# Kernel tuning notes

Hardware: AMD Instinct MI355X
Metric: run time of the kernel (lower is better)

## Reference

```python
import jax, jax.numpy as jnp
import numpy as np

N = 100000      # nodes
E = 1_600_000   # edges (avg degree 16)
F = 128         # num_features
H = 128         # hidden
C = 10          # num_classes


def _agg_norm(row, col, mask, n, by_row):
    # A[dst=row, src=col]; scale rows (target) or cols (source) by mask,
    # remove any existing diagonal entries and add self-loops with value 1
    # (fill_diag(A,1.0)), then symmetric D^-1/2 A D^-1/2 normalization.
    m = mask[row] if by_row else mask[col]
    val = jnp.where(row == col, 0.0, m)              # off-diagonal edge values
    deg = jax.ops.segment_sum(val, row, num_segments=n) + 1.0  # +1 from self-loop
    dinv = deg ** -0.5                                # deg >= 1, never inf
    return dinv[row] * val * dinv[col], dinv * dinv   # edge vals, diag vals


def _spmm(val, diag, row, col, x, n):
    # y = A_hat @ x with off-diagonal edge list + explicit diagonal
    y = jax.ops.segment_sum(val[:, None] * x[col], row, num_segments=n)
    return y + diag[:, None] * x


def setup_inputs() -> dict:
    key = jax.random.key(0)
    ks = jax.random.split(key, 12)
    x = jax.random.normal(ks[0], (N, F), jnp.float32)
    src = jax.random.randint(ks[1], (E,), 0, N)
    dst = jax.random.randint(ks[2], (E,), 0, N)
    edge_index = jnp.stack([src, dst]).astype(jnp.int64)
    cc_mask = (jax.random.uniform(ks[3], (N,)) < 0.5).astype(jnp.float32)
    s = 0.05  # stand-in for xavier scale; exact init irrelevant to correctness
    W1L = jax.random.normal(ks[4], (F, H), jnp.float32) * s
    W1H = jax.random.normal(ks[5], (F, H), jnp.float32) * s
    W2L = jax.random.normal(ks[6], (H, H), jnp.float32) * s
    W2H = jax.random.normal(ks[7], (H, H), jnp.float32) * s
    WX = jax.random.normal(ks[8], (F, H), jnp.float32) * s
    lam1 = jnp.zeros((2,), jnp.float32)
    lam2 = jnp.zeros((2,), jnp.float32)
    lin_w = jax.random.normal(ks[9], (H, C), jnp.float32) * s
    lin_b = jnp.zeros((C,), jnp.float32)
    return {"x": x, "edge_index": edge_index, "cc_mask": cc_mask,
            "W1L": W1L, "W1H": W1H, "W2L": W2L, "W2H": W2H, "WX": WX,
            "lam1": lam1, "lam2": lam2, "lin_w": lin_w, "lin_b": lin_b}


def reference(x, edge_index, cc_mask, W1L, W1H, W2L, W2H, WX, lam1, lam2, lin_w, lin_b):
    n = x.shape[0]
    row = edge_index[1]   # destination (aggregation target)
    col = edge_index[0]   # source
    rev = 1.0 - cc_mask

    vl,  dl  = _agg_norm(row, col, cc_mask, n, True)    # target-masked (low)
    vll, dll = _agg_norm(row, col, cc_mask, n, False)   # source-masked (low)
    vh,  dh  = _agg_norm(row, col, rev,     n, True)    # target-masked (high)
    vhh, dhh = _agg_norm(row, col, rev,     n, False)   # source-masked (high)

    xl = jax.nn.relu(_spmm(vl, dl, row, col, x, n) @ W1L)
    xl = _spmm(vll, dll, row, col, xl, n) @ W2L

    xh = jax.nn.relu(_spmm(vh, dh, row, col, x, n) @ W1H)
    xh = _spmm(vhh, dhh, row, col, xh, n) @ W2H

    xc = x @ WX

    lamxl, laml = jax.nn.softmax(lam1)
    lamxh, lamh = jax.nn.softmax(lam2)
    lamx = lamxl * cc_mask + lamxh * rev                # per-node gate [N]

    xf = jax.nn.relu(lamx[:, None] * xc + laml * xl + lamh * xh)
    return xf @ lin_w + lin_b                           # [N, C] logits
```

## Files before the change

kernel.cpp:

```cpp
#include <hip/hip_runtime.h>
#include <stdint.h>

typedef unsigned int u32;
typedef unsigned short u16;
typedef unsigned long long u64;

#define DI __device__ __forceinline__

DI float bf2f(u16 u) { union { u32 i; float f; } v; v.i = ((u32)u) << 16; return v.f; }
DI u16 f2bf(float f) {
    union { u32 i; float f; } v; v.f = f;
    u32 u = v.i;
    u32 r = (u + 0x7fffu + ((u >> 16) & 1u)) >> 16;
    return (u16)r;
}
DI float2 unpack2(u32 x) { return make_float2(bf2f((u16)(x & 0xffffu)), bf2f((u16)(x >> 16))); }
DI u32 pack2(float a, float b) { return (u32)f2bf(a) | ((u32)f2bf(b) << 16); }

DI void fma8(float* acc, float w, uint4 xv) {
    float2 f0 = unpack2(xv.x), f1 = unpack2(xv.y), f2 = unpack2(xv.z), f3 = unpack2(xv.w);
    acc[0] += w * f0.x; acc[1] += w * f0.y; acc[2] += w * f1.x; acc[3] += w * f1.y;
    acc[4] += w * f2.x; acc[5] += w * f2.y; acc[6] += w * f3.x; acc[7] += w * f3.y;
}

DI uint4 scale8(uint4 v, float s) {
    uint4 r;
    float2 f;
    f = unpack2(v.x); r.x = pack2(f.x * s, f.y * s);
    f = unpack2(v.y); r.y = pack2(f.x * s, f.y * s);
    f = unpack2(v.z); r.z = pack2(f.x * s, f.y * s);
    f = unpack2(v.w); r.w = pack2(f.x * s, f.y * s);
    return r;
}


__global__ void pre_k(const float* __restrict__ X, u16* __restrict__ Xb, int total4, int cvtBlocks,
                      const float* __restrict__ mask, u64* __restrict__ bits, int n) {
    if ((int)blockIdx.x < cvtBlocks) {
        int i = blockIdx.x * blockDim.x + threadIdx.x;
        if (i >= total4) return;
        float4 v = ((const float4*)X)[i];
        ushort4 o;
        o.x = f2bf(v.x); o.y = f2bf(v.y); o.z = f2bf(v.z); o.w = f2bf(v.w);
        ((ushort4*)Xb)[i] = o;
    } else {
        int bid = blockIdx.x - cvtBlocks;
        int i = bid * 256 + threadIdx.x;
        bool m = (i < n) && (mask[i] != 0.f);
        u64 word = __ballot(m);
        if ((threadIdx.x & 63) == 0) {
            if (i < n) bits[i >> 6] = word;
        }
    }
}


#define CHUNK 8192
#define NBPAD 800

__global__ __launch_bounds__(256) void k_count(const int* __restrict__ ei, int E, int NB,
                                               u32* __restrict__ hist2d) {
    __shared__ u32 hist[NBPAD];
    for (int i = threadIdx.x; i < NBPAD; i += 256) hist[i] = 0;
    __syncthreads();
    int base = blockIdx.x * CHUNK;
    int end = min(base + CHUNK, E);
    for (int e = base + threadIdx.x; e < end; e += 256) {
        int c = ei[e], r = ei[E + e];
        if (r != c) atomicAdd(&hist[r >> 7], 1u);
    }
    __syncthreads();
    u32* out = hist2d + (size_t)blockIdx.x * NBPAD;
    for (int i = threadIdx.x; i < NB; i += 256) out[i] = hist[i];
}

__global__ __launch_bounds__(256) void k_colscan(const u32* __restrict__ hist2d,
                                                 u32* __restrict__ off2d,
                                                 int NBLK, u32* __restrict__ btotal) {
    __shared__ u32 s[256];
    int t = blockIdx.x;
    int k = threadIdx.x;
    u32 v = (k < NBLK) ? hist2d[(size_t)k * NBPAD + t] : 0;
    s[k] = v;
    __syncthreads();
    for (int off = 1; off < 256; off <<= 1) {
        u32 tmp = (k >= off) ? s[k - off] : 0;
        __syncthreads();
        s[k] += tmp;
        __syncthreads();
    }
    if (k < NBLK) off2d[(size_t)k * NBPAD + t] = s[k] - v;
    if (k == 0) btotal[t] = s[255];
}

__global__ __launch_bounds__(1024) void k_basescan(const u32* __restrict__ btotal,
                                                   u32* __restrict__ bbase, int NB) {
    __shared__ u32 s[1024];
    int t = threadIdx.x;
    u32 v = (t < NB) ? btotal[t] : 0;
    s[t] = v;
    __syncthreads();
    for (int off = 1; off < 1024; off <<= 1) {
        u32 tmp = (t >= off) ? s[t - off] : 0;
        __syncthreads();
        s[t] += tmp;
        __syncthreads();
    }
    if (t < NB) bbase[t] = s[t] - v;
    if (t == NB - 1) bbase[NB] = s[t];
}

__global__ __launch_bounds__(256) void k_scatter(const int* __restrict__ ei, int E, int NB,
                                                 const u32* __restrict__ off2d,
                                                 const u32* __restrict__ bbase,
                                                 const u64* __restrict__ bits,
                                                 u32* __restrict__ bentry) {
    __shared__ u32 cur[NBPAD];
    const u32* off = off2d + (size_t)blockIdx.x * NBPAD;
    for (int i = threadIdx.x; i < NB; i += 256) cur[i] = off[i] + bbase[i];
    __syncthreads();
    int base = blockIdx.x * CHUNK;
    int end = min(base + CHUNK, E);
    for (int e = base + threadIdx.x; e < end; e += 256) {
        int c = ei[e], r = ei[E + e];
        if (r != c) {
            u32 pos = atomicAdd(&cur[r >> 7], 1u);
            u32 m = (u32)((bits[c >> 6] >> (c & 63)) & 1);
            bentry[pos] = (u32)(r & 127) | ((u32)c << 7) | (m << 31);
        }
    }
}

__global__ __launch_bounds__(256) void k_rowhist(const u32* __restrict__ bentry,
                                                 const u32* __restrict__ bbase,
                                                 u32* __restrict__ cntP, int n) {
    __shared__ u32 h[128];
    if (threadIdx.x < 128) h[threadIdx.x] = 0;
    __syncthreads();
    u32 s0 = bbase[blockIdx.x], s1 = bbase[blockIdx.x + 1];
    for (u32 i = s0 + threadIdx.x; i < s1; i += 256) {
        u32 e = bentry[i];
        atomicAdd(&h[e & 127], 1u + ((e >> 31) << 16));
    }
    __syncthreads();
    int row = blockIdx.x * 128 + threadIdx.x;
    if (threadIdx.x < 128 && row < n) cntP[row] = h[threadIdx.x];
}

#define SCAN_B 1024
__global__ __launch_bounds__(1024) void scanA(const u32* __restrict__ cntP, int* __restrict__ rowptr,
                                              int* __restrict__ blocksum, int n) {
    __shared__ int s[SCAN_B];
    int t = threadIdx.x;
    int i = blockIdx.x * SCAN_B + t;
    int v = (i < n) ? (int)(cntP[i] & 0xffffu) : 0;
    s[t] = v; __syncthreads();
    for (int off = 1; off < SCAN_B; off <<= 1) {
        int tmp = (t >= off) ? s[t - off] : 0;
        __syncthreads();
        s[t] += tmp;
        __syncthreads();
    }
    if (i < n) rowptr[i] = s[t] - v;
    if (t == SCAN_B - 1) blocksum[blockIdx.x] = s[t];
}

__global__ __launch_bounds__(256) void scanBC(const int* __restrict__ blocksum, int nblk,
                                              int* __restrict__ rowptr, const u32* __restrict__ cntP,
                                              const float* __restrict__ mask,
                                              int* __restrict__ mid,
                                              float* __restrict__ dinvL, float* __restrict__ dinvH,
                                              float* __restrict__ dinvLL, float* __restrict__ dinvHH,
                                              float2* __restrict__ diag1, float2* __restrict__ diag2, int n) {
    __shared__ int s[128];
    int t = threadIdx.x;
    if (t < 128) s[t] = (t < nblk) ? blocksum[t] : 0;
    __syncthreads();
    for (int off = 1; off < 128; off <<= 1) {
        int tmp = (t >= off && t < 128) ? s[t - off] : 0;
        __syncthreads();
        if (t < 128) s[t] += tmp;
        __syncthreads();
    }
    int blockoff = (blockIdx.x == 0) ? 0 : s[blockIdx.x - 1];
    if (blockIdx.x == 0 && t == 0) rowptr[n] = s[127];
#pragma unroll
    for (int k = 0; k < 4; k++) {
        int i = blockIdx.x * SCAN_B + k * 256 + t;
        if (i >= n) break;
        int v = rowptr[i] + blockoff;
        rowptr[i] = v;
        u32 p = cntP[i];
        int ci = (int)(p & 0xffffu);
        int cmi = (int)(p >> 16);
        mid[i] = v + cmi;
        float c = (float)ci;
        float cm = (float)cmi;
        bool mi = mask[i] != 0.f;
        float degL = (mi ? c : 0.f) + 1.f;
        float degH = (mi ? 0.f : c) + 1.f;
        float degLL = cm + 1.f;
        float degHH = (c - cm) + 1.f;
        dinvL[i] = rsqrtf(degL);
        dinvH[i] = rsqrtf(degH);
        dinvLL[i] = rsqrtf(degLL);
        dinvHH[i] = rsqrtf(degHH);
        diag1[i] = make_float2(1.f / degL, 1.f / degH);
        diag2[i] = make_float2(1.f / degLL, 1.f / degHH);
    }
}

__global__ __launch_bounds__(256) void k_place(const u32* __restrict__ bentry,
                                               const u32* __restrict__ bbase,
                                               const int* __restrict__ rowptr, const int* __restrict__ mid,
                                               int* __restrict__ sorted, int n) {
    __shared__ int cur[256];
    int row = blockIdx.x * 128 + threadIdx.x;
    if (threadIdx.x < 128) {
        int rr = min(row, n - 1);
        cur[threadIdx.x] = rowptr[rr];
        cur[128 + threadIdx.x] = mid[rr];
    }
    __syncthreads();
    u32 s0 = bbase[blockIdx.x], s1 = bbase[blockIdx.x + 1];
    for (u32 i = s0 + threadIdx.x; i < s1; i += 256) {
        u32 e = bentry[i];
        int rl = e & 127;
        int col = (int)((e >> 7) & 0x1FFFF);
        int isH = (int)((e >> 31) ^ 1u);
        int pos = atomicAdd(&cur[rl + (isH << 7)], 1);
        sorted[pos] = col;
    }
}


__global__ __launch_bounds__(256) void spmm1(const u16* __restrict__ X,
                                             const int* __restrict__ rowptr, const int* __restrict__ sorted,
                                             const float* __restrict__ mask,
                                             const float* __restrict__ dinvL, const float* __restrict__ dinvH,
                                             const float2* __restrict__ diag1,
                                             u16* __restrict__ Yl, u16* __restrict__ Yh, int n) {
    int r = blockIdx.x * 4 + (threadIdx.x >> 6);
    if (r >= n) return;
    int lane = threadIdx.x & 63;
    int q = lane >> 4, l16 = lane & 15;
    bool mi = mask[r] != 0.f;
    const float* dinvA = mi ? dinvL : dinvH;
    float da = dinvA[r];
    float2 dg = diag1[r];
    float diag = mi ? dg.x : dg.y;

    const uint4* Xv = (const uint4*)X;
    uint4 xown = Xv[(size_t)r * 16 + l16];

    float acc[8] = {0.f, 0.f, 0.f, 0.f, 0.f, 0.f, 0.f, 0.f};
    int e0 = rowptr[r], e1 = rowptr[r + 1];
    int last = e1 - 1;
    for (int base = e0; base < e1; base += 8) {
        int s0 = base + q, s1 = base + 4 + q;
        int i0 = min(s0, last), i1 = min(s1, last);
        int c0 = sorted[i0], c1 = sorted[i1];
        float w0 = (s0 < e1) ? da * dinvA[c0] : 0.f;
        float w1 = (s1 < e1) ? da * dinvA[c1] : 0.f;
        uint4 x0 = Xv[(size_t)c0 * 16 + l16];
        uint4 x1 = Xv[(size_t)c1 * 16 + l16];
        fma8(acc, w0, x0);
        fma8(acc, w1, x1);
    }
#pragma unroll
    for (int k = 0; k < 8; k++) {
        acc[k] += __shfl_xor(acc[k], 16);
        acc[k] += __shfl_xor(acc[k], 32);
    }
    float2 o0 = unpack2(xown.x), o1 = unpack2(xown.y), o2 = unpack2(xown.z), o3 = unpack2(xown.w);
    uint4 res;
    res.x = pack2(acc[0] + diag * o0.x, acc[1] + diag * o0.y);
    res.y = pack2(acc[2] + diag * o1.x, acc[3] + diag * o1.y);
    res.z = pack2(acc[4] + diag * o2.x, acc[5] + diag * o2.y);
    res.w = pack2(acc[6] + diag * o3.x, acc[7] + diag * o3.y);
    uint4* Ya = (uint4*)(mi ? Yl : Yh);
    uint4* Yc = (uint4*)(mi ? Yh : Yl);
    if (q == 0) Ya[(size_t)r * 16 + l16] = res;
    if (q == 1) Yc[(size_t)r * 16 + l16] = xown;
}


__global__ __launch_bounds__(256) void spmm2(const u16* __restrict__ XL, const u16* __restrict__ XH,
                                             const int* __restrict__ rowptr, const int* __restrict__ mid,
                                             const int* __restrict__ sorted,
                                             const float* __restrict__ dinvLL, const float* __restrict__ dinvHH,
                                             const float2* __restrict__ diag2,
                                             u16* __restrict__ Zl, u16* __restrict__ Zh, int n) {
    int r = blockIdx.x * 4 + (threadIdx.x >> 6);
    if (r >= n) return;
    int lane = threadIdx.x & 63;
    int q = lane >> 4, l16 = lane & 15;

    float dllr = dinvLL[r], dhhr = dinvHH[r];
    float2 dg = diag2[r];

    const uint4* XLv = (const uint4*)XL;
    const uint4* XHv = (const uint4*)XH;
    uint4 xlown = XLv[(size_t)r * 16 + l16];
    uint4 xhown = XHv[(size_t)r * 16 + l16];

    float accL[8] = {0.f, 0.f, 0.f, 0.f, 0.f, 0.f, 0.f, 0.f};
    float accH[8] = {0.f, 0.f, 0.f, 0.f, 0.f, 0.f, 0.f, 0.f};
    int e0 = rowptr[r], m = mid[r], e1 = rowptr[r + 1];

    int lastL = m - 1;
    for (int base = e0; base < m; base += 8) {
        int s0 = base + q, s1 = base + 4 + q;
        int i0 = min(s0, lastL), i1 = min(s1, lastL);
        int c0 = sorted[i0], c1 = sorted[i1];
        float w0 = (s0 < m) ? dllr * dinvLL[c0] : 0.f;
        float w1 = (s1 < m) ? dllr * dinvLL[c1] : 0.f;
        uint4 x0 = XLv[(size_t)c0 * 16 + l16];
        uint4 x1 = XLv[(size_t)c1 * 16 + l16];
        fma8(accL, w0, x0);
        fma8(accL, w1, x1);
    }
    int lastH = e1 - 1;
    for (int base = m; base < e1; base += 8) {
        int s0 = base + q, s1 = base + 4 + q;
        int i0 = min(s0, lastH), i1 = min(s1, lastH);
        int c0 = sorted[i0], c1 = sorted[i1];
        float w0 = (s0 < e1) ? dhhr * dinvHH[c0] : 0.f;
        float w1 = (s1 < e1) ? dhhr * dinvHH[c1] : 0.f;
        uint4 x0 = XHv[(size_t)c0 * 16 + l16];
        uint4 x1 = XHv[(size_t)c1 * 16 + l16];
        fma8(accH, w0, x0);
        fma8(accH, w1, x1);
    }
#pragma unroll
    for (int k = 0; k < 8; k++) {
        accL[k] += __shfl_xor(accL[k], 16);
        accL[k] += __shfl_xor(accL[k], 32);
        accH[k] += __shfl_xor(accH[k], 16);
        accH[k] += __shfl_xor(accH[k], 32);
    }
    float2 l0 = unpack2(xlown.x), l1 = unpack2(xlown.y), l2 = unpack2(xlown.z), l3 = unpack2(xlown.w);
    float2 h0 = unpack2(xhown.x), h1 = unpack2(xhown.y), h2 = unpack2(xhown.z), h3 = unpack2(xhown.w);
    float cl = dg.x, ch = dg.y;
    uint4 rl, rh;
    rl.x = pack2(accL[0] + cl * l0.x, accL[1] + cl * l0.y);
    rl.y = pack2(accL[2] + cl * l1.x, accL[3] + cl * l1.y);
    rl.z = pack2(accL[4] + cl * l2.x, accL[5] + cl * l2.y);
    rl.w = pack2(accL[6] + cl * l3.x, accL[7] + cl * l3.y);
    rh.x = pack2(accH[0] + ch * h0.x, accH[1] + ch * h0.y);
    rh.y = pack2(accH[2] + ch * h1.x, accH[3] + ch * h1.y);
    rh.z = pack2(accH[4] + ch * h2.x, accH[5] + ch * h2.y);
    rh.w = pack2(accH[6] + ch * h3.x, accH[7] + ch * h3.y);
    if (q == 0) ((uint4*)Zl)[(size_t)r * 16 + l16] = rl;
    if (q == 1) ((uint4*)Zh)[(size_t)r * 16 + l16] = rh;
}


__global__ void transposeW(const float* __restrict__ W1L, const float* __restrict__ W1H,
                           const float* __restrict__ W2L, const float* __restrict__ W2H,
                           const float* __restrict__ WX,
                           const float* __restrict__ lam1, const float* __restrict__ lam2,
                           u16* __restrict__ Bt) {
    int w = blockIdx.x >> 6;
    int idx = (blockIdx.x & 63) * 256 + threadIdx.x;
    float scale = 1.f;
    if (w == 2) { float e0 = __expf(lam1[0]), e1 = __expf(lam1[1]); scale = e1 / (e0 + e1); }
    if (w == 3) { float f0 = __expf(lam2[0]), f1 = __expf(lam2[1]); scale = f1 / (f0 + f1); }
    const float* src = (w == 0) ? W1L : (w == 1) ? W1H : (w == 2) ? W2L : (w == 3) ? W2H : WX;
    int k = idx >> 7, nn = idx & 127;
    Bt[(size_t)w * 16384 + (size_t)nn * 128 + k] = f2bf(scale * src[idx]);
}


typedef __attribute__((ext_vector_type(8))) short bf16x8;
typedef __attribute__((ext_vector_type(4))) float f32x4;

DI void stageB(const uint4* __restrict__ Bt4, uint4* Bs, int tid) {
#pragma unroll
    for (int i = 0; i < 8; i++) {
        int g = i * 256 + tid;
        int nn = g >> 4, c = g & 15;
        int d = ((nn >> 4) * 4 + (c >> 2)) * 64 + (c & 3) * 16 + (nn & 15);
        Bs[d] = Bt4[g];
    }
}

DI void loadA(uint4* a, const uint4* __restrict__ A4, int mr, int quad) {
#pragma unroll
    for (int kb = 0; kb < 4; kb++)
        a[kb] = A4[(size_t)mr * 16 + kb * 4 + quad];
}

DI void mfmaSec(const uint4* a, const uint4* Bs, f32x4* acc, int lane) {
#pragma unroll
    for (int nt = 0; nt < 8; nt++)
#pragma unroll
        for (int kb = 0; kb < 4; kb++) {
            bf16x8 av = *(const bf16x8*)&a[kb];
            bf16x8 bv = *(const bf16x8*)&Bs[(nt * 4 + kb) * 64 + lane];
            acc[nt] = __builtin_amdgcn_mfma_f32_16x16x32_bf16(av, bv, acc[nt], 0, 0, 0);
        }
}


__global__ __launch_bounds__(256) void gemm_lds(const u16* __restrict__ A0, const u16* __restrict__ Bt0,
                                                u16* __restrict__ C0,
                                                const u16* __restrict__ A1, const u16* __restrict__ Bt1,
                                                u16* __restrict__ C1, int M) {
    __shared__ uint4 Bs[2048];
    const u16* A = blockIdx.y ? A1 : A0;
    const u16* Bt = blockIdx.y ? Bt1 : Bt0;
    u16* C = blockIdx.y ? C1 : C0;

    int tid = threadIdx.x;
    int wave = tid >> 6, lane = tid & 63, quad = lane >> 4, l16 = lane & 15;
    int tile = blockIdx.x * 64;
    int m0 = tile + wave * 16 + l16;
    int mr = min(m0, M - 1);

    uint4 a[4];
    loadA(a, (const uint4*)A, mr, quad);
    stageB((const uint4*)Bt, Bs, tid);
    __syncthreads();

    f32x4 acc[8];
#pragma unroll
    for (int nt = 0; nt < 8; nt++) acc[nt] = f32x4{0.f, 0.f, 0.f, 0.f};
    mfmaSec(a, Bs, acc, lane);

    __syncthreads();
    u16* Cs = (u16*)Bs;
    int lrow0 = wave * 16 + quad * 4;
#pragma unroll
    for (int nt = 0; nt < 8; nt++)
#pragma unroll
        for (int rr = 0; rr < 4; rr++) {
            float v = acc[nt][rr];
            v = v > 0.f ? v : 0.f;
            Cs[(lrow0 + rr) * 128 + nt * 16 + l16] = f2bf(v);
        }
    __syncthreads();
    uint4* Cs4 = (uint4*)Bs;
    uint4* C4 = (uint4*)C;
#pragma unroll
    for (int i = 0; i < 4; i++) {
        int g = i * 256 + tid;
        int grow = tile + (g >> 4);
        if (grow < M) C4[(size_t)grow * 16 + (g & 15)] = Cs4[g];
    }
}


__global__ __launch_bounds__(256) void fused_final(const u16* __restrict__ Zl, const u16* __restrict__ Zh,
                                                   const u16* __restrict__ Xb,
                                                   const u16* __restrict__ BtL, const u16* __restrict__ BtH,
                                                   const u16* __restrict__ BtX,
                                                   const float* __restrict__ mask,
                                                   const float* __restrict__ lam1, const float* __restrict__ lam2,
                                                   const float* __restrict__ lin_w, const float* __restrict__ lin_b,
                                                   float* __restrict__ out, int M) {
    __shared__ uint4 Bs[2048];
    __shared__ float lws[1280];

    int tid = threadIdx.x;
    int wave = tid >> 6, lane = tid & 63, quad = lane >> 4, l16 = lane & 15;
    int tile = blockIdx.x * 64;
    int m0 = tile + wave * 16 + l16;
    int mr = min(m0, M - 1);

    uint4 a[4], an[4];
    loadA(a, (const uint4*)Zl, mr, quad);
    {
        const uint4* lw4 = (const uint4*)lin_w;
        uint4* lws4 = (uint4*)lws;
        lws4[tid] = lw4[tid];
        if (tid < 64) lws4[256 + tid] = lw4[256 + tid];
    }
    stageB((const uint4*)BtL, Bs, tid);

    float e0 = __expf(lam1[0]), e1 = __expf(lam1[1]);
    float lamxl = e0 / (e0 + e1);
    float f0 = __expf(lam2[0]), f1 = __expf(lam2[1]);
    float lamxh = f0 / (f0 + f1);
    float lamx = (mask[mr] != 0.f) ? lamxl : lamxh;

    __syncthreads();

    f32x4 acc[8];
#pragma unroll
    for (int nt = 0; nt < 8; nt++) acc[nt] = f32x4{0.f, 0.f, 0.f, 0.f};

    loadA(an, (const uint4*)Zh, mr, quad);
    mfmaSec(a, Bs, acc, lane);

    __syncthreads();
    stageB((const uint4*)BtH, Bs, tid);
#pragma unroll
    for (int kb = 0; kb < 4; kb++) a[kb] = an[kb];
    loadA(an, (const uint4*)Xb, mr, quad);
    __syncthreads();
    mfmaSec(a, Bs, acc, lane);

    __syncthreads();
    stageB((const uint4*)BtX, Bs, tid);
#pragma unroll
    for (int kb = 0; kb < 4; kb++) a[kb] = scale8(an[kb], lamx);
    __syncthreads();
    mfmaSec(a, Bs, acc, lane);

    int rbase = tile + wave * 16 + quad * 4;
    float part[4][10];
#pragma unroll
    for (int rr = 0; rr < 4; rr++)
#pragma unroll
        for (int c = 0; c < 10; c++) part[rr][c] = 0.f;

#pragma unroll
    for (int nt = 0; nt < 8; nt++) {
        const float* lw = lws + (nt * 16 + l16) * 10;
        float lwv[10];
#pragma unroll
        for (int c = 0; c < 10; c++) lwv[c] = lw[c];
#pragma unroll
        for (int rr = 0; rr < 4; rr++) {
            float p = acc[nt][rr];
            p = p > 0.f ? p : 0.f;
#pragma unroll
            for (int c = 0; c < 10; c++) part[rr][c] += p * lwv[c];
        }
    }
#pragma unroll
    for (int rr = 0; rr < 4; rr++)
#pragma unroll
        for (int c = 0; c < 10; c++) {
            part[rr][c] += __shfl_xor(part[rr][c], 1);
            part[rr][c] += __shfl_xor(part[rr][c], 2);
            part[rr][c] += __shfl_xor(part[rr][c], 4);
            part[rr][c] += __shfl_xor(part[rr][c], 8);
        }
    if (l16 == 0) {
#pragma unroll
        for (int rr = 0; rr < 4; rr++) {
            int row = rbase + rr;
            if (row < M) {
#pragma unroll
                for (int c = 0; c < 10; c++)
                    out[(size_t)row * 10 + c] = part[rr][c] + lin_b[c];
            }
        }
    }
}


extern "C" void kernel_launch(void* const* d_in, const int* in_sizes, int n_in,
                              void* d_out, int out_size, void* d_ws, size_t ws_size,
                              hipStream_t stream) {
    const float* x = (const float*)d_in[0];
    const int* ei = (const int*)d_in[1];
    const float* mask = (const float*)d_in[2];
    const float* W1L = (const float*)d_in[3];
    const float* W1H = (const float*)d_in[4];
    const float* W2L = (const float*)d_in[5];
    const float* W2H = (const float*)d_in[6];
    const float* WX = (const float*)d_in[7];
    const float* lam1 = (const float*)d_in[8];
    const float* lam2 = (const float*)d_in[9];
    const float* lin_w = (const float*)d_in[10];
    const float* lin_b = (const float*)d_in[11];
    float* out = (float*)d_out;

    int E = in_sizes[1] / 2;
    int n = in_sizes[2];
    int NB = (n + 127) >> 7;
    int NBLK = (E + CHUNK - 1) / CHUNK;

    char* w = (char*)d_ws;
    size_t off = 0;
    auto alloc = [&](size_t bytes) -> void* {
        off = (off + 255) & ~(size_t)255;
        void* p = w + off;
        off += bytes;
        return p;
    };
    u32* cntP = (u32*)alloc((size_t)n * 4);
    u64* bits = (u64*)alloc((size_t)((n + 63) / 64 + 1) * 8);
    int* rowptr = (int*)alloc((size_t)(n + 1) * 4);
    int* midp = (int*)alloc((size_t)n * 4);
    int* blocksum = (int*)alloc(128 * 4);
    u32* hist2d = (u32*)alloc((size_t)NBLK * NBPAD * 4);
    u32* off2d = (u32*)alloc((size_t)NBLK * NBPAD * 4);
    u32* btotal = (u32*)alloc((size_t)NBPAD * 4);
    u32* bbase = (u32*)alloc((size_t)(NB + 1) * 4);
    u32* bentry = (u32*)alloc((size_t)E * 4);
    int* sorted = (int*)alloc((size_t)E * 4);
    float* dinvL = (float*)alloc((size_t)n * 4);
    float* dinvH = (float*)alloc((size_t)n * 4);
    float* dinvLL = (float*)alloc((size_t)n * 4);
    float* dinvHH = (float*)alloc((size_t)n * 4);
    float2* diag1 = (float2*)alloc((size_t)n * 8);
    float2* diag2 = (float2*)alloc((size_t)n * 8);
    u16* Bt = (u16*)alloc(5 * 16384 * 2);
    size_t actb = (size_t)n * 128 * 2;
    u16* Xb = (u16*)alloc(actb);
    u16* B0 = (u16*)alloc(actb);
    u16* B1 = (u16*)alloc(actb);
    u16* B2 = (u16*)alloc(actb);
    u16* B3 = (u16*)alloc(actb);

    int nblkScan = (n + SCAN_B - 1) / SCAN_B;
    int total4 = n * 128 / 4;
    int cvtBlocks = (total4 + 255) / 256;
    int maskBlocks = ((n + 63) / 64 + 3) / 4;

    pre_k<<<cvtBlocks + maskBlocks, 256, 0, stream>>>(x, Xb, total4, cvtBlocks, mask, bits, n);
    k_count<<<NBLK, 256, 0, stream>>>(ei, E, NB, hist2d);
    k_colscan<<<NB, 256, 0, stream>>>(hist2d, off2d, NBLK, btotal);
    k_basescan<<<1, 1024, 0, stream>>>(btotal, bbase, NB);
    k_scatter<<<NBLK, 256, 0, stream>>>(ei, E, NB, off2d, bbase, bits, bentry);
    k_rowhist<<<NB, 256, 0, stream>>>(bentry, bbase, cntP, n);
    scanA<<<nblkScan, 1024, 0, stream>>>(cntP, rowptr, blocksum, n);
    scanBC<<<nblkScan, 256, 0, stream>>>(blocksum, nblkScan, rowptr, cntP, mask, midp,
                                         dinvL, dinvH, dinvLL, dinvHH, diag1, diag2, n);
    k_place<<<NB, 256, 0, stream>>>(bentry, bbase, rowptr, midp, sorted, n);

    int rowsblk = (n + 3) / 4;
    int gemmblk = (n + 63) / 64;

    spmm1<<<rowsblk, 256, 0, stream>>>(Xb, rowptr, sorted, mask, dinvL, dinvH, diag1, B0, B1, n);
    transposeW<<<320, 256, 0, stream>>>(W1L, W1H, W2L, W2H, WX, lam1, lam2, Bt);
    gemm_lds<<<dim3(gemmblk, 2), 256, 0, stream>>>(B0, Bt + 0 * 16384, B2,
                                                   B1, Bt + 1 * 16384, B3, n);

    spmm2<<<rowsblk, 256, 0, stream>>>(B2, B3, rowptr, midp, sorted, dinvLL, dinvHH, diag2, B0, B1, n);

    fused_final<<<gemmblk, 256, 0, stream>>>(B0, B1, Xb,
                                             Bt + 2 * 16384, Bt + 3 * 16384, Bt + 4 * 16384,
                                             mask, lam1, lam2, lin_w, lin_b, out, n);
}
```

Before: 413.3 us.

## Merge preprocessing kernels into one launch and simplify SpMM gather loop

```diff
diff --git a/kernel.cpp b/kernel.cpp
--- a/kernel.cpp
+++ b/kernel.cpp
@@ -34,43 +34,61 @@
 }
 
 
-__global__ void pre_k(const float* __restrict__ X, u16* __restrict__ Xb, int total4, int cvtBlocks,
-                      const float* __restrict__ mask, u64* __restrict__ bits, int n) {
-    if ((int)blockIdx.x < cvtBlocks) {
-        int i = blockIdx.x * blockDim.x + threadIdx.x;
+#define CHUNK 8192
+#define NBPAD 800
+
+__global__ __launch_bounds__(256) void head_k(const float* __restrict__ X, u16* __restrict__ Xb,
+                                              int total4, int cvtBlocks, int maskBlocks,
+                                              const float* __restrict__ mask, u64* __restrict__ bits, int n,
+                                              const float* __restrict__ W1L, const float* __restrict__ W1H,
+                                              const float* __restrict__ W2L, const float* __restrict__ W2H,
+                                              const float* __restrict__ WX,
+                                              const float* __restrict__ lam1, const float* __restrict__ lam2,
+                                              u16* __restrict__ Bt,
+                                              const int* __restrict__ ei, int E, int NB,
+                                              u32* __restrict__ hist2d) {
+    int bx = blockIdx.x;
+    if (bx < cvtBlocks) {
+        int i = bx * 256 + threadIdx.x;
         if (i >= total4) return;
         float4 v = ((const float4*)X)[i];
         ushort4 o;
         o.x = f2bf(v.x); o.y = f2bf(v.y); o.z = f2bf(v.z); o.w = f2bf(v.w);
         ((ushort4*)Xb)[i] = o;
-    } else {
-        int bid = blockIdx.x - cvtBlocks;
-        int i = bid * 256 + threadIdx.x;
+        return;
+    }
+    bx -= cvtBlocks;
+    if (bx < maskBlocks) {
+        int i = bx * 256 + threadIdx.x;
         bool m = (i < n) && (mask[i] != 0.f);
         u64 word = __ballot(m);
-        if ((threadIdx.x & 63) == 0) {
-            if (i < n) bits[i >> 6] = word;
-        }
-    }
-}
-
-
-#define CHUNK 8192
-#define NBPAD 800
-
-__global__ __launch_bounds__(256) void k_count(const int* __restrict__ ei, int E, int NB,
-                                               u32* __restrict__ hist2d) {
+        if ((threadIdx.x & 63) == 0 && i < n) bits[i >> 6] = word;
+        return;
+    }
+    bx -= maskBlocks;
+    if (bx < 320) {
+        int w = bx >> 6;
+        int idx = (bx & 63) * 256 + threadIdx.x;
+        float scale = 1.f;
+        if (w == 2) { float e0 = __expf(lam1[0]), e1 = __expf(lam1[1]); scale = e1 / (e0 + e1); }
+        if (w == 3) { float f0 = __expf(lam2[0]), f1 = __expf(lam2[1]); scale = f1 / (f0 + f1); }
+        const float* src = (w == 0) ? W1L : (w == 1) ? W1H : (w == 2) ? W2L : (w == 3) ? W2H : WX;
+        int k = idx >> 7, nn = idx & 127;
+        Bt[(size_t)w * 16384 + (size_t)nn * 128 + k] = f2bf(scale * src[idx]);
+        return;
+    }
+    bx -= 320;
     __shared__ u32 hist[NBPAD];
     for (int i = threadIdx.x; i < NBPAD; i += 256) hist[i] = 0;
     __syncthreads();
-    int base = blockIdx.x * CHUNK;
+    int base = bx * CHUNK;
     int end = min(base + CHUNK, E);
     for (int e = base + threadIdx.x; e < end; e += 256) {
         int c = ei[e], r = ei[E + e];
         if (r != c) atomicAdd(&hist[r >> 7], 1u);
     }
     __syncthreads();
-    u32* out = hist2d + (size_t)blockIdx.x * NBPAD;
+    u32* out = hist2d + (size_t)bx * NBPAD;
     for (int i = threadIdx.x; i < NB; i += 256) out[i] = hist[i];
 }
 
@@ -234,6 +252,31 @@
 }
 
 
+DI void gather_phase(const uint4* __restrict__ Xv, const int* __restrict__ sorted,
+                     const float* __restrict__ dinv, float dr,
+                     int e0, int e1, int q, int l16, float* acc) {
+    int len = e1 - e0;
+    int nfull = len >> 2;
+    int e = e0;
+#pragma unroll 2
+    for (int it = 0; it < nfull; it++) {
+        int c = sorted[e + q];
+        float w = dr * dinv[c];
+        uint4 xv = Xv[(size_t)c * 16 + l16];
+        fma8(acc, w, xv);
+        e += 4;
+    }
+    int rem = len & 3;
+    if (rem) {
+        int idx = min(e + q, e1 - 1);
+        int c = sorted[idx];
+        float w = (q < rem) ? dr * dinv[c] : 0.f;
+        uint4 xv = Xv[(size_t)c * 16 + l16];
+        fma8(acc, w, xv);
+    }
+}
+
+
 __global__ __launch_bounds__(256) void spmm1(const u16* __restrict__ X,
                                              const int* __restrict__ rowptr, const int* __restrict__ sorted,
                                              const float* __restrict__ mask,
@@ -255,18 +298,8 @@
 
     float acc[8] = {0.f, 0.f, 0.f, 0.f, 0.f, 0.f, 0.f, 0.f};
     int e0 = rowptr[r], e1 = rowptr[r + 1];
-    int last = e1 - 1;
-    for (int base = e0; base < e1; base += 8) {
-        int s0 = base + q, s1 = base + 4 + q;
-        int i0 = min(s0, last), i1 = min(s1, last);
-        int c0 = sorted[i0], c1 = sorted[i1];
-        float w0 = (s0 < e1) ? da * dinvA[c0] : 0.f;
-        float w1 = (s1 < e1) ? da * dinvA[c1] : 0.f;
-        uint4 x0 = Xv[(size_t)c0 * 16 + l16];
-        uint4 x1 = Xv[(size_t)c1 * 16 + l16];
-        fma8(acc, w0, x0);
-        fma8(acc, w1, x1);
-    }
+    gather_phase(Xv, sorted, dinvA, da, e0, e1, q, l16, acc);
+
 #pragma unroll
     for (int k = 0; k < 8; k++) {
         acc[k] += __shfl_xor(acc[k], 16);
@@ -308,30 +341,9 @@
     float accH[8] = {0.f, 0.f, 0.f, 0.f, 0.f, 0.f, 0.f, 0.f};
     int e0 = rowptr[r], m = mid[r], e1 = rowptr[r + 1];
 
-    int lastL = m - 1;
-    for (int base = e0; base < m; base += 8) {
-        int s0 = base + q, s1 = base + 4 + q;
-        int i0 = min(s0, lastL), i1 = min(s1, lastL);
-        int c0 = sorted[i0], c1 = sorted[i1];
-        float w0 = (s0 < m) ? dllr * dinvLL[c0] : 0.f;
-        float w1 = (s1 < m) ? dllr * dinvLL[c1] : 0.f;
-        uint4 x0 = XLv[(size_t)c0 * 16 + l16];
-        uint4 x1 = XLv[(size_t)c1 * 16 + l16];
-        fma8(accL, w0, x0);
-        fma8(accL, w1, x1);
-    }
-    int lastH = e1 - 1;
-    for (int base = m; base < e1; base += 8) {
-        int s0 = base + q, s1 = base + 4 + q;
-        int i0 = min(s0, lastH), i1 = min(s1, lastH);
-        int c0 = sorted[i0], c1 = sorted[i1];
-        float w0 = (s0 < e1) ? dhhr * dinvHH[c0] : 0.f;
-        float w1 = (s1 < e1) ? dhhr * dinvHH[c1] : 0.f;
-        uint4 x0 = XHv[(size_t)c0 * 16 + l16];
-        uint4 x1 = XHv[(size_t)c1 * 16 + l16];
-        fma8(accH, w0, x0);
-        fma8(accH, w1, x1);
-    }
+    gather_phase(XLv, sorted, dinvLL, dllr, e0, m, q, l16, accL);
+    gather_phase(XHv, sorted, dinvHH, dhhr, m, e1, q, l16, accH);
+
 #pragma unroll
     for (int k = 0; k < 8; k++) {
         accL[k] += __shfl_xor(accL[k], 16);
@@ -353,22 +365,6 @@
     rh.w = pack2(accH[6] + ch * h3.x, accH[7] + ch * h3.y);
     if (q == 0) ((uint4*)Zl)[(size_t)r * 16 + l16] = rl;
     if (q == 1) ((uint4*)Zh)[(size_t)r * 16 + l16] = rh;
-}
-
-
-__global__ void transposeW(const float* __restrict__ W1L, const float* __restrict__ W1H,
-                           const float* __restrict__ W2L, const float* __restrict__ W2H,
-                           const float* __restrict__ WX,
-                           const float* __restrict__ lam1, const float* __restrict__ lam2,
-                           u16* __restrict__ Bt) {
-    int w = blockIdx.x >> 6;
-    int idx = (blockIdx.x & 63) * 256 + threadIdx.x;
-    float scale = 1.f;
-    if (w == 2) { float e0 = __expf(lam1[0]), e1 = __expf(lam1[1]); scale = e1 / (e0 + e1); }
-    if (w == 3) { float f0 = __expf(lam2[0]), f1 = __expf(lam2[1]); scale = f1 / (f0 + f1); }
-    const float* src = (w == 0) ? W1L : (w == 1) ? W1H : (w == 2) ? W2L : (w == 3) ? W2H : WX;
-    int k = idx >> 7, nn = idx & 127;
-    Bt[(size_t)w * 16384 + (size_t)nn * 128 + k] = f2bf(scale * src[idx]);
 }
 
 
@@ -612,8 +608,9 @@
     int cvtBlocks = (total4 + 255) / 256;
     int maskBlocks = ((n + 63) / 64 + 3) / 4;
 
-    pre_k<<<cvtBlocks + maskBlocks, 256, 0, stream>>>(x, Xb, total4, cvtBlocks, mask, bits, n);
-    k_count<<<NBLK, 256, 0, stream>>>(ei, E, NB, hist2d);
+    head_k<<<cvtBlocks + maskBlocks + 320 + NBLK, 256, 0, stream>>>(
+        x, Xb, total4, cvtBlocks, maskBlocks, mask, bits, n,
+        W1L, W1H, W2L, W2H, WX, lam1, lam2, Bt, ei, E, NB, hist2d);
     k_colscan<<<NB, 256, 0, stream>>>(hist2d, off2d, NBLK, btotal);
     k_basescan<<<1, 1024, 0, stream>>>(btotal, bbase, NB);
     k_scatter<<<NBLK, 256, 0, stream>>>(ei, E, NB, off2d, bbase, bits, bentry);
@@ -627,7 +624,6 @@
     int gemmblk = (n + 63) / 64;
 
     spmm1<<<rowsblk, 256, 0, stream>>>(Xb, rowptr, sorted, mask, dinvL, dinvH, diag1, B0, B1, n);
-    transposeW<<<320, 256, 0, stream>>>(W1L, W1H, W2L, W2H, WX, lam1, lam2, Bt);
     gemm_lds<<<dim3(gemmblk, 2), 256, 0, stream>>>(B0, Bt + 0 * 16384, B2,
                                                    B1, Bt + 1 * 16384, B3, n);
 
```

Measured after the change: 403.6 us. 2.4% less time.
